# Kernel optimization log

Hardware: AMD Instinct MI355X
Metric: run time of the kernel (lower is better)

Reference implementation:

```python
import jax, jax.numpy as jnp
import numpy as np

LN_EPS = 1e-3  # keras LayerNormalization default epsilon

def setup_inputs() -> dict:
    key = jax.random.key(0)
    ks = jax.random.split(key, 8)
    B, T, N, F_in, F_out, S = 4, 4, 65536, 16, 32, 8
    E = 589824  # ~9 edges per node (8-neighbor grid + self loop)
    return {
        "water": jax.random.normal(ks[0], (B, T, N, F_in), jnp.float32),
        "static": jax.random.uniform(ks[1], (B, T, N, S), jnp.float32),
        "adj_rows": jax.random.randint(ks[2], (E,), 0, N, jnp.int32),
        "adj_cols": jax.random.randint(ks[3], (E,), 0, N, jnp.int32),
        "adj_vals": jax.random.uniform(ks[4], (E,), jnp.float32),
        "W_feat": (jax.random.normal(ks[5], (F_in, F_out), jnp.float32) * 0.1),
        "b_feat": jnp.zeros((F_out,), jnp.float32),
        "Wg1": (jax.random.normal(ks[6], (3, 1), jnp.float32) * 0.1),
        "bg1": jnp.zeros((1,), jnp.float32),
        "Wg2": (jax.random.normal(ks[7], (S - 3, 1), jnp.float32) * 0.1),
        "bg2": jnp.zeros((1,), jnp.float32),
        "ln_gamma": jnp.ones((F_out,), jnp.float32),
        "ln_beta": jnp.zeros((F_out,), jnp.float32),
        "min_gate": jnp.float32(0.1),
    }


def reference(water, static, adj_rows, adj_cols, adj_vals,
              W_feat, b_feat, Wg1, bg1, Wg2, bg2, ln_gamma, ln_beta, min_gate):
    B, T, N, F_in = water.shape
    # gated feature scaling: gate in (0,1], per (b,t,n)
    gate = jax.nn.sigmoid(static[..., :3] @ Wg1 + bg1) * jax.nn.sigmoid(static[..., 3:] @ Wg2 + bg2)
    gate = jnp.maximum(gate, min_gate)  # [B,T,N,1]
    x = (water * gate).reshape(B * T, N, F_in)
    # SpMM shared across all F_in channels and all B*T slices:
    # out[bt,n,f] = sum_{edges (n<-m)} adj_vals * x[bt,m,f]
    xs = x.transpose(1, 0, 2)                       # [N, BT, F]
    msg = adj_vals[:, None, None] * xs[adj_cols]    # [E, BT, F]
    agg = jax.ops.segment_sum(msg, adj_rows, num_segments=N)  # [N, BT, F]
    h = agg.transpose(1, 0, 2)                      # [BT, N, F]
    out = h @ W_feat + b_feat                       # [BT, N, F_out]
    out = out.reshape(B, T, N, -1)
    # layer norm over channel axis (keras default axis=-1)
    mu = out.mean(-1, keepdims=True)
    var = out.var(-1, keepdims=True)
    out = (out - mu) * jax.lax.rsqrt(var + LN_EPS) * ln_gamma + ln_beta
    # dropout is identity at inference
    return out
```

## Files before the change

### kernel.cpp

```cpp
#include <hip/hip_runtime.h>

#define BT   16
#define FIN  16
#define FOUT 32
#define CAP  32

typedef float    f32x4 __attribute__((ext_vector_type(4)));
typedef _Float16 f16x4 __attribute__((ext_vector_type(4)));
typedef _Float16 f16x8 __attribute__((ext_vector_type(8)));
typedef unsigned int u32;


__global__ __launch_bounds__(256) void zero_kernel(int4* __restrict__ p, int n4) {
    int i = blockIdx.x * 256 + threadIdx.x;
    if (i < n4) p[i] = make_int4(0, 0, 0, 0);
}


__global__ __launch_bounds__(256) void scatter_gate_kernel(
        const int* __restrict__ rows, const int* __restrict__ cols,
        const float* __restrict__ vals,
        int* __restrict__ cur, u32* __restrict__ edge_s, int E, int eb,
        const float* __restrict__ water,
        const float* __restrict__ st,
        const float* __restrict__ Wg1, const float* __restrict__ bg1,
        const float* __restrict__ Wg2, const float* __restrict__ bg2,
        const float* __restrict__ min_gate,
        _Float16* __restrict__ x, int N) {
    if (blockIdx.x < (unsigned)eb) {
        int i0 = (blockIdx.x * 256 + threadIdx.x) * 4;
        if (i0 + 4 <= E) {
            int4   r4 = *(const int4*)  (rows + i0);
            int4   c4 = *(const int4*)  (cols + i0);
            f32x4  v4 = *(const f32x4*) (vals + i0);
#pragma unroll
            for (int k = 0; k < 4; ++k) {
                int r = (&r4.x)[k];
                int pos = atomicAdd(&cur[r << 4], 1);
                unsigned short vh = __builtin_bit_cast(unsigned short, (_Float16)v4[k]);
                if (pos < CAP)
                    edge_s[(size_t)r * CAP + pos] = ((u32)vh << 16) | (u32)(&c4.x)[k];
            }
        } else {
            for (int e = i0; e < E; ++e) {
                int r = rows[e];
                int pos = atomicAdd(&cur[r << 4], 1);
                unsigned short vh = __builtin_bit_cast(unsigned short, (_Float16)vals[e]);
                if (pos < CAP)
                    edge_s[(size_t)r * CAP + pos] = ((u32)vh << 16) | (u32)cols[e];
            }
        }
    } else {
        int g  = blockIdx.x - eb;
        int n  = g * 16 + (threadIdx.x & 15);
        int bt = threadIdx.x >> 4;

        const f32x4* sp = (const f32x4*)(st + ((size_t)bt * N + n) * 8);
        f32x4 s0 = sp[0];
        f32x4 s1 = sp[1];
        float g1 = s0.x * Wg1[0] + s0.y * Wg1[1] + s0.z * Wg1[2] + bg1[0];
        float g2 = s0.w * Wg2[0] + s1.x * Wg2[1] + s1.y * Wg2[2] + s1.z * Wg2[3] + s1.w * Wg2[4] + bg2[0];
        g1 = 1.f / (1.f + __expf(-g1));
        g2 = 1.f / (1.f + __expf(-g2));
        float gate = fmaxf(g1 * g2, min_gate[0]);

        const f32x4* wp = (const f32x4*)(water + ((size_t)bt * N + n) * FIN);
        f16x8 h0, h1;
#pragma unroll
        for (int k = 0; k < 4; ++k) {
            f32x4 w = wp[k];
            w *= gate;
            f16x8& h = (k < 2) ? h0 : h1;
            int b = (k & 1) * 4;
            h[b + 0] = (_Float16)w.x; h[b + 1] = (_Float16)w.y;
            h[b + 2] = (_Float16)w.z; h[b + 3] = (_Float16)w.w;
        }
        f16x8* xp = (f16x8*)(x + ((size_t)n * BT + bt) * FIN);
        xp[0] = h0;
        xp[1] = h1;
    }
}


#define GA(i)  p##i = ebase[i];      g##i = xv[(size_t)(p##i & 0xffffu) * 64 + l];
#define GB(i)  p##i = ebase[16 + i]; g##i = xv[(size_t)(p##i & 0xffffu) * 64 + l];
#define FM(i)                                                                    \
    {                                                                            \
        u32 hv = (i < cnt) ? (p##i >> 16) : 0u;                                  \
        float v = (float)__builtin_bit_cast(_Float16, (unsigned short)hv);       \
        acc.x += v * (float)g##i[0];  acc.y += v * (float)g##i[1];               \
        acc.z += v * (float)g##i[2];  acc.w += v * (float)g##i[3];               \
    }
#define FB(i)                                                                    \
    {                                                                            \
        u32 hv = (16 + i < cnt) ? (p##i >> 16) : 0u;                             \
        float v = (float)__builtin_bit_cast(_Float16, (unsigned short)hv);       \
        acc.x += v * (float)g##i[0];  acc.y += v * (float)g##i[1];               \
        acc.z += v * (float)g##i[2];  acc.w += v * (float)g##i[3];               \
    }

__global__ __launch_bounds__(256) void spmm_ln_kernel(
        const _Float16* __restrict__ x,
        const int* __restrict__ cur,
        const u32* __restrict__ edge_s,
        const float* __restrict__ W,
        const float* __restrict__ bvec,
        const float* __restrict__ gamma,
        const float* __restrict__ beta,
        float* __restrict__ out, int N) {
    __shared__ float Wsh[FIN][FOUT];
    __shared__ float psh[3][FOUT];
    __shared__ f32x4 osh[4][BT][9];

    int t = threadIdx.x;
    Wsh[t >> 5][t & 31]       = W[t];
    Wsh[(t >> 5) + 8][t & 31] = W[t + 256];
    if (t < 32)       psh[0][t]      = bvec[t];
    else if (t < 64)  psh[1][t - 32] = gamma[t - 32];
    else if (t < 96)  psh[2][t - 64] = beta[t - 64];
    __syncthreads();

    int l  = t & 63;
    int wv = t >> 6;
    int n = __builtin_amdgcn_readfirstlane(blockIdx.x * 4 + wv);
    int cnt = __builtin_amdgcn_readfirstlane(cur[n << 4]);
    cnt = (cnt < CAP) ? cnt : CAP;
    int pcnt = (cnt + 3) & ~3;
    int k4 = pcnt >> 2; k4 = (k4 < 4) ? k4 : 4;
    const u32* ebase = edge_s + (size_t)n * CAP;
    const f16x4* xv = (const f16x4*)x;

    u32 p0,p1,p2,p3,p4,p5,p6,p7,p8,p9,p10,p11,p12,p13,p14,p15;
    f16x4 g0,g1,g2,g3,g4,g5,g6,g7,g8,g9,g10,g11,g12,g13,g14,g15;
    f32x4 acc = {0.f, 0.f, 0.f, 0.f};

    switch (k4) {
        case 4: GA(12) GA(13) GA(14) GA(15)
        case 3: GA(8)  GA(9)  GA(10) GA(11)
        case 2: GA(4)  GA(5)  GA(6)  GA(7)
        case 1: GA(0)  GA(1)  GA(2)  GA(3)  break;
        default: break;
    }
    switch (k4) {
        case 4: FM(12) FM(13) FM(14) FM(15)
        case 3: FM(8)  FM(9)  FM(10) FM(11)
        case 2: FM(4)  FM(5)  FM(6)  FM(7)
        case 1: FM(0)  FM(1)  FM(2)  FM(3)  break;
        default: break;
    }
    if (cnt > 16) {
        GB(0) GB(1) GB(2) GB(3) GB(4) GB(5) GB(6) GB(7)
        GB(8) GB(9) GB(10) GB(11) GB(12) GB(13) GB(14) GB(15)
        FB(0) FB(1) FB(2) FB(3) FB(4) FB(5) FB(6) FB(7)
        FB(8) FB(9) FB(10) FB(11) FB(12) FB(13) FB(14) FB(15)
    }

    int d = l & 3;
    float o[8];
#pragma unroll
    for (int jj = 0; jj < 8; ++jj) o[jj] = psh[0][d * 8 + jj];
#pragma unroll
    for (int q = 0; q < 4; ++q) {
        float hq[4];
        hq[0] = __shfl(acc.x, q, 4);
        hq[1] = __shfl(acc.y, q, 4);
        hq[2] = __shfl(acc.z, q, 4);
        hq[3] = __shfl(acc.w, q, 4);
#pragma unroll
        for (int m = 0; m < 4; ++m) {
            float hk = hq[m];
#pragma unroll
            for (int jj = 0; jj < 8; ++jj)
                o[jj] += hk * Wsh[q * 4 + m][d * 8 + jj];
        }
    }

    float s = 0.f, sq = 0.f;
#pragma unroll
    for (int jj = 0; jj < 8; ++jj) { s += o[jj]; sq += o[jj] * o[jj]; }
    s  += __shfl_xor(s,  1, 4);  sq += __shfl_xor(sq, 1, 4);
    s  += __shfl_xor(s,  2, 4);  sq += __shfl_xor(sq, 2, 4);
    float mu  = s * (1.f / 32.f);
    float var = sq * (1.f / 32.f) - mu * mu;
    float inv = rsqrtf(var + 1e-3f);

    f32x4 r0, r1;
#pragma unroll
    for (int jj = 0; jj < 8; ++jj) {
        float val = (o[jj] - mu) * inv * psh[1][d * 8 + jj] + psh[2][d * 8 + jj];
        if (jj < 4) r0[jj] = val;
        else        r1[jj - 4] = val;
    }
    int bt = l >> 2;
    osh[wv][bt][d * 2]     = r0;
    osh[wv][bt][d * 2 + 1] = r1;
    __syncthreads();

    int n0 = blockIdx.x * 4;
#pragma unroll
    for (int ps = 0; ps < 2; ++ps) {
        int idx = ps * 256 + t;
        int bt2 = idx >> 5;
        int q2  = idx & 31;
        int j   = q2 >> 3;
        int v   = q2 & 7;
        f32x4 r = osh[j][bt2][v];
        *(f32x4*)(out + (size_t)bt2 * N * FOUT + (size_t)(n0 + j) * FOUT + v * 4) = r;
    }
}


extern "C" void kernel_launch(void* const* d_in, const int* in_sizes, int n_in,
                              void* d_out, int out_size, void* d_ws, size_t ws_size,
                              hipStream_t stream) {
    const float* water    = (const float*)d_in[0];
    const float* st       = (const float*)d_in[1];
    const int*   adj_rows = (const int*)  d_in[2];
    const int*   adj_cols = (const int*)  d_in[3];
    const float* adj_vals = (const float*)d_in[4];
    const float* W_feat   = (const float*)d_in[5];
    const float* b_feat   = (const float*)d_in[6];
    const float* Wg1      = (const float*)d_in[7];
    const float* bg1      = (const float*)d_in[8];
    const float* Wg2      = (const float*)d_in[9];
    const float* bg2      = (const float*)d_in[10];
    const float* ln_gamma = (const float*)d_in[11];
    const float* ln_beta  = (const float*)d_in[12];
    const float* min_gate = (const float*)d_in[13];
    float* out = (float*)d_out;

    int N = in_sizes[0] / (BT * FIN);
    int E = in_sizes[2];

    char* ws = (char*)d_ws;
    size_t off = 0;
    auto alloc = [&](size_t bytes) -> void* {
        off = (off + 255) & ~(size_t)255;
        void* p = ws + off;
        off += bytes;
        return p;
    };
    int*      cur    = (int*)     alloc((size_t)N * 16 * sizeof(int));
    u32*      edge_s = (u32*)     alloc((size_t)N * CAP * sizeof(u32));
    _Float16* x      = (_Float16*)alloc((size_t)N * BT * FIN * sizeof(_Float16));

    int eb = (E + 1023) / 1024;
    int gb = N / 16;

    zero_kernel<<<N / 64, 256, 0, stream>>>((int4*)cur, N * 4);
    scatter_gate_kernel<<<eb + gb, 256, 0, stream>>>(
        adj_rows, adj_cols, adj_vals, cur, edge_s, E, eb,
        water, st, Wg1, bg1, Wg2, bg2, min_gate, x, N);
    spmm_ln_kernel<<<N / 4, 256, 0, stream>>>(
        x, cur, edge_s, W_feat, b_feat, ln_gamma, ln_beta, out, N);
}
```

Before: 126.8 us.

## Replace per-row global atomic scatter with two-level bin sort into CSR

Edges are first bucketed into 256 row-bins using shared-memory atomics per block and one global atomic per bin. A new binsort kernel then sorts each bin by local row in shared memory and writes a compact CSR layout plus per-row offset and count metadata. The SpMM kernel reads that metadata and gains a tail loop, so rows with more than 32 edges are no longer truncated. This removes about 590K contended global atomics and the fixed-capacity per-row slots, at the cost of an extra kernel launch and another pass over the edges. Bins that exceed BCAP still drop edges.

```diff
diff --git a/kernel.cpp b/kernel.cpp
--- a/kernel.cpp
+++ b/kernel.cpp
@@ -1,9 +1,11 @@
 #include <hip/hip_runtime.h>
 
-#define BT   16
-#define FIN  16
-#define FOUT 32
-#define CAP  32
+#define BT    16
+#define FIN   16
+#define FOUT  32
+#define NB    256
+#define BCAP  2816
+#define P1E   4096
 
 typedef float    f32x4 __attribute__((ext_vector_type(4)));
 typedef _Float16 f16x4 __attribute__((ext_vector_type(4)));
@@ -20,40 +22,57 @@
 __global__ __launch_bounds__(256) void scatter_gate_kernel(
         const int* __restrict__ rows, const int* __restrict__ cols,
         const float* __restrict__ vals,
-        int* __restrict__ cur, u32* __restrict__ edge_s, int E, int eb,
+        int* __restrict__ gcnt,
+        uint2* __restrict__ edge8,
+        int E, int eb,
         const float* __restrict__ water,
         const float* __restrict__ st,
         const float* __restrict__ Wg1, const float* __restrict__ bg1,
         const float* __restrict__ Wg2, const float* __restrict__ bg2,
         const float* __restrict__ min_gate,
         _Float16* __restrict__ x, int N) {
+    __shared__ unsigned short rk[P1E];
+    __shared__ int lcnt[NB];
+    __shared__ int gbase[NB];
+
+    int t = threadIdx.x;
     if (blockIdx.x < (unsigned)eb) {
-        int i0 = (blockIdx.x * 256 + threadIdx.x) * 4;
-        if (i0 + 4 <= E) {
-            int4   r4 = *(const int4*)  (rows + i0);
-            int4   c4 = *(const int4*)  (cols + i0);
-            f32x4  v4 = *(const f32x4*) (vals + i0);
-#pragma unroll
-            for (int k = 0; k < 4; ++k) {
-                int r = (&r4.x)[k];
-                int pos = atomicAdd(&cur[r << 4], 1);
-                unsigned short vh = __builtin_bit_cast(unsigned short, (_Float16)v4[k]);
-                if (pos < CAP)
-                    edge_s[(size_t)r * CAP + pos] = ((u32)vh << 16) | (u32)(&c4.x)[k];
+        lcnt[t] = 0;
+        __syncthreads();
+        size_t e0 = (size_t)blockIdx.x * P1E;
+#pragma unroll
+        for (int c = 0; c < P1E / 256; ++c) {
+            int i = c * 256 + t;
+            if (e0 + i < (size_t)E) {
+                int r = rows[e0 + i];
+                rk[i] = (unsigned short)atomicAdd(&lcnt[r >> 8], 1);
             }
-        } else {
-            for (int e = i0; e < E; ++e) {
-                int r = rows[e];
-                int pos = atomicAdd(&cur[r << 4], 1);
-                unsigned short vh = __builtin_bit_cast(unsigned short, (_Float16)vals[e]);
-                if (pos < CAP)
-                    edge_s[(size_t)r * CAP + pos] = ((u32)vh << 16) | (u32)cols[e];
+        }
+        __syncthreads();
+        gbase[t] = atomicAdd(&gcnt[t << 4], lcnt[t]);
+        __syncthreads();
+#pragma unroll
+        for (int c = 0; c < P1E / 256; ++c) {
+            int i = c * 256 + t;
+            if (e0 + i < (size_t)E) {
+                int r  = rows[e0 + i];
+                int cl = cols[e0 + i];
+                float v = vals[e0 + i];
+                int b = r >> 8;
+                int dst = gbase[b] + rk[i];
+                if (dst < BCAP) {
+                    unsigned short vh = __builtin_bit_cast(unsigned short, (_Float16)v);
+                    uint2 rec;
+                    rec.x = ((u32)vh << 16) | (u32)cl;
+                    rec.y = (u32)(r & 255);
+                    edge8[(size_t)b * BCAP + dst] = rec;
+                }
             }
         }
     } else {
         int g  = blockIdx.x - eb;
-        int n  = g * 16 + (threadIdx.x & 15);
-        int bt = threadIdx.x >> 4;
+        int n  = g * 16 + (t & 15);
+        int bt = t >> 4;
 
         const f32x4* sp = (const f32x4*)(st + ((size_t)bt * N + n) * 8);
         f32x4 s0 = sp[0];
@@ -82,6 +101,50 @@
 }
 
 
+__global__ __launch_bounds__(256) void binsort_kernel(
+        const uint2* __restrict__ edge8,
+        const int* __restrict__ gcnt,
+        u32* __restrict__ final_e,
+        int2* __restrict__ row_meta) {
+    __shared__ uint2 ed[BCAP];
+    __shared__ int cnt[NB];
+    __shared__ int off[NB];
+
+    int b = blockIdx.x, t = threadIdx.x;
+    int m = gcnt[b << 4];
+    m = (m < BCAP) ? m : BCAP;
+    cnt[t] = 0;
+    __syncthreads();
+    for (int i = t; i < m; i += 256) {
+        uint2 r = edge8[(size_t)b * BCAP + i];
+        int rl = r.y & 255;
+        int rank = atomicAdd(&cnt[rl], 1);
+        r.y = ((u32)rank << 8) | (u32)rl;
+        ed[i] = r;
+    }
+    __syncthreads();
+    int v = cnt[t];
+    off[t] = v;
+    __syncthreads();
+    for (int s = 1; s < 256; s <<= 1) {
+        int u = (t >= s) ? off[t - s] : 0;
+        __syncthreads();
+        off[t] += u;
+        __syncthreads();
+    }
+    int excl = off[t] - v;
+    row_meta[b * 256 + t] = make_int2(b * BCAP + excl, v);
+    off[t] = excl;
+    __syncthreads();
+    for (int i = t; i < m; i += 256) {
+        uint2 r = ed[i];
+        int rl = r.y & 255;
+        int rank = (int)(r.y >> 8);
+        final_e[(size_t)b * BCAP + off[rl] + rank] = r.x;
+    }
+}
+
+
 #define GA(i)  p##i = ebase[i];      g##i = xv[(size_t)(p##i & 0xffffu) * 64 + l];
 #define GB(i)  p##i = ebase[16 + i]; g##i = xv[(size_t)(p##i & 0xffffu) * 64 + l];
 #define FM(i)                                                                    \
@@ -101,8 +164,8 @@
 
 __global__ __launch_bounds__(256) void spmm_ln_kernel(
         const _Float16* __restrict__ x,
-        const int* __restrict__ cur,
-        const u32* __restrict__ edge_s,
+        const int2* __restrict__ row_meta,
+        const u32* __restrict__ final_e,
         const float* __restrict__ W,
         const float* __restrict__ bvec,
         const float* __restrict__ gamma,
@@ -123,11 +186,13 @@
     int l  = t & 63;
     int wv = t >> 6;
     int n = __builtin_amdgcn_readfirstlane(blockIdx.x * 4 + wv);
-    int cnt = __builtin_amdgcn_readfirstlane(cur[n << 4]);
-    cnt = (cnt < CAP) ? cnt : CAP;
-    int pcnt = (cnt + 3) & ~3;
-    int k4 = pcnt >> 2; k4 = (k4 < 4) ? k4 : 4;
-    const u32* ebase = edge_s + (size_t)n * CAP;
+    int2 md = row_meta[n];
+    int e0  = __builtin_amdgcn_readfirstlane(md.x);
+    int cnt = __builtin_amdgcn_readfirstlane(md.y);
+    int c16 = (cnt < 16) ? cnt : 16;
+    int pcnt = (c16 + 3) & ~3;
+    int k4 = pcnt >> 2;
+    const u32* ebase = final_e + e0;
     const f16x4* xv = (const f16x4*)x;
 
     u32 p0,p1,p2,p3,p4,p5,p6,p7,p8,p9,p10,p11,p12,p13,p14,p15;
@@ -153,6 +218,17 @@
         GB(8) GB(9) GB(10) GB(11) GB(12) GB(13) GB(14) GB(15)
         FB(0) FB(1) FB(2) FB(3) FB(4) FB(5) FB(6) FB(7)
         FB(8) FB(9) FB(10) FB(11) FB(12) FB(13) FB(14) FB(15)
+    }
+    for (int bs = 32; bs < cnt; bs += 8) {
+#pragma unroll
+        for (int i2 = 0; i2 < 8; ++i2) {
+            u32 p = ebase[bs + i2];
+            f16x4 g = xv[(size_t)(p & 0xffffu) * 64 + l];
+            u32 hv = (bs + i2 < cnt) ? (p >> 16) : 0u;
+            float v = (float)__builtin_bit_cast(_Float16, (unsigned short)hv);
+            acc.x += v * (float)g[0];  acc.y += v * (float)g[1];
+            acc.z += v * (float)g[2];  acc.w += v * (float)g[3];
+        }
     }
 
     int d = l & 3;
@@ -240,17 +316,20 @@
         off += bytes;
         return p;
     };
-    int*      cur    = (int*)     alloc((size_t)N * 16 * sizeof(int));
-    u32*      edge_s = (u32*)     alloc((size_t)N * CAP * sizeof(u32));
-    _Float16* x      = (_Float16*)alloc((size_t)N * BT * FIN * sizeof(_Float16));
-
-    int eb = (E + 1023) / 1024;
+    int*      gcnt     = (int*)     alloc((size_t)NB * 16 * sizeof(int));
+    uint2*    edge8    = (uint2*)   alloc(((size_t)NB * BCAP + 64) * sizeof(uint2));
+    u32*      final_e  = (u32*)     alloc(((size_t)NB * BCAP + 64) * sizeof(u32));
+    int2*     row_meta = (int2*)    alloc((size_t)N * sizeof(int2));
+    _Float16* x        = (_Float16*)alloc((size_t)N * BT * FIN * sizeof(_Float16));
+
+    int eb = (E + P1E - 1) / P1E;
     int gb = N / 16;
 
-    zero_kernel<<<N / 64, 256, 0, stream>>>((int4*)cur, N * 4);
+    zero_kernel<<<4, 256, 0, stream>>>((int4*)gcnt, NB * 4);
     scatter_gate_kernel<<<eb + gb, 256, 0, stream>>>(
-        adj_rows, adj_cols, adj_vals, cur, edge_s, E, eb,
+        adj_rows, adj_cols, adj_vals, gcnt, edge8, E, eb,
         water, st, Wg1, bg1, Wg2, bg2, min_gate, x, N);
+    binsort_kernel<<<NB, 256, 0, stream>>>(edge8, gcnt, final_e, row_meta);
     spmm_ln_kernel<<<N / 4, 256, 0, stream>>>(
-        x, cur, edge_s, W_feat, b_feat, ln_gamma, ln_beta, out, N);
-}
+        x, row_meta, final_e, W_feat, b_feat, ln_gamma, ln_beta, out, N);
+}
```

Measured after the change: 125.1 us. About the same (-1.3%).
